# Performance work log

Measured on AMD Instinct MI355X. Metric: run time of the kernel, lower is better.

## Reference

```python
import jax, jax.numpy as jnp
import numpy as np

B, T, C = 8, 2048, 1024
HEAD = 64

def setup_inputs() -> dict:
    key = jax.random.key(0)
    k1, k2, k3, k4 = jax.random.split(key, 4)
    x = jax.random.normal(k1, (B, T, C), dtype=jnp.float32)
    # nn.Linear(n_embed, head_size, bias=False): y = x @ W^T; store as [C, HEAD] for x @ W
    scale = 1.0 / np.sqrt(C)
    Wq = jax.random.normal(k2, (C, HEAD), dtype=jnp.float32) * scale
    Wk = jax.random.normal(k3, (C, HEAD), dtype=jnp.float32) * scale
    Wv = jax.random.normal(k4, (C, HEAD), dtype=jnp.float32) * scale
    return {"x": x, "Wq": Wq, "Wk": Wk, "Wv": Wv}

def reference(x, Wq, Wk, Wv):
    Bx, Tx, Cx = x.shape
    q = x @ Wq            # [B,T,H]
    k = x @ Wk            # [B,T,H]
    v = x @ Wv            # [B,T,H]
    # NOTE: original scales by C**-0.5 (embedding dim), not head_size**-0.5
    aff = jnp.einsum('bqh,bkh->bqk', q, k) * (Cx ** -0.5)  # [B,T,T]
    causal = jnp.tril(jnp.ones((Tx, Tx), dtype=bool))
    aff = jnp.where(causal, aff, -jnp.inf)
    probs = jax.nn.softmax(aff, axis=-1)
    # dropout p=0.0 (eval): identity
    return jnp.einsum('bqk,bkh->bqh', probs, v)
```

## Files before the change

### kernel.cpp

```cpp
#include <hip/hip_runtime.h>
#include <hip/hip_bf16.h>

typedef __attribute__((ext_vector_type(8))) short bf16x8;
typedef __attribute__((ext_vector_type(4))) float f32x4;
typedef __attribute__((ext_vector_type(4))) int i32x4;

#define LOG2E 1.4426950408889634f

static __device__ __forceinline__ unsigned int f2bfu(float f) {
    return (unsigned int)__builtin_bit_cast(unsigned short, __float2bfloat16(f));
}
static __device__ __forceinline__ unsigned int pack2(float lo, float hi) {
    return (f2bfu(hi) << 16) | f2bfu(lo);
}
static __device__ __forceinline__ unsigned short f2bf(float f) {
    return __builtin_bit_cast(unsigned short, __float2bfloat16(f));
}
static __device__ __forceinline__ void gload16(const void* g, void* l) {
    __builtin_amdgcn_global_load_lds(
        (const __attribute__((address_space(1))) unsigned int*)g,
        (__attribute__((address_space(3))) unsigned int*)l,
        16, 0, 0);
}

__global__ __launch_bounds__(256) void wtrans_kernel(
    const float* __restrict__ Wq, const float* __restrict__ Wk,
    const float* __restrict__ Wv, unsigned short* __restrict__ Wts)
{
    const int part = blockIdx.x;
    const int t    = blockIdx.y;
    const int c    = part * 256 + threadIdx.x;
    const int n    = c >> 3;
    const int mat  = n >> 6;
    const int nl   = n & 63;
    const int k0   = t * 64 + (c & 7) * 8;
    const float* W = (mat == 0) ? Wq : ((mat == 1) ? Wk : Wv);
    const float scale = (mat == 0) ? 0.03125f : 1.0f;
    unsigned int s[8];
#pragma unroll
    for (int j = 0; j < 8; ++j)
        s[j] = (unsigned int)f2bf(W[(size_t)(k0 + j) * 64 + nl] * scale);
    i32x4 pk;
    pk[0] = (int)(s[0] | (s[1] << 16));
    pk[1] = (int)(s[2] | (s[3] << 16));
    pk[2] = (int)(s[4] | (s[5] << 16));
    pk[3] = (int)(s[6] | (s[7] << 16));
    *(i32x4*)(Wts + (size_t)t * 12288 + (size_t)c * 8) = pk;
}

__global__ __launch_bounds__(256, 2) void proj_kernel(
    const float* __restrict__ x, const unsigned short* __restrict__ Wts,
    unsigned short* __restrict__ Qb, unsigned short* __restrict__ Kp,
    unsigned short* __restrict__ Vp)
{
    __shared__ __align__(16) unsigned short sA[2][32][72];
    __shared__ __align__(16) unsigned short sBlin[2][12288];
    __shared__ __align__(16) unsigned short sVT[64][48];
    __shared__ __align__(16) unsigned short sK[32][72];

    const int tid  = threadIdx.x;
    const int w    = tid >> 6;
    const int wm   = w >> 1;
    const int wn   = w & 1;
    const int lane = tid & 63;
    const int r    = lane & 15;
    const int g    = lane >> 4;
    const int xv   = r & 7;
    const int mbase = blockIdx.x * 32;

    const int arow = tid >> 3;
    const int acb  = (tid & 7) * 8;
    const float* xptr = x + (size_t)(mbase + arow) * 1024 + acb;

    f32x4 acc[6];
#pragma unroll
    for (int i = 0; i < 6; ++i) acc[i] = (f32x4)0.0f;

    float4 XAa0, XAa1, XAb0, XAb1;

#define LOADX(S0, S1, t_) do { \
        const float* xp = xptr + (size_t)(t_) * 64; \
        S0 = *(const float4*)(xp);  S1 = *(const float4*)(xp + 4); \
    } while (0)

#define GLOADB(t_, buf) do { \
        const unsigned short* wtb = Wts + (size_t)(t_) * 12288; \
        _Pragma("unroll") \
        for (int i = 0; i < 6; ++i) { \
            const int sslot = (w * 6 + i) * 64 + lane; \
            const int ssrc  = sslot ^ ((sslot >> 3) & 7); \
            gload16(wtb + (size_t)ssrc * 8, &sBlin[buf][(size_t)(w * 6 + i) * 512]); \
        } \
    } while (0)

#define STOREA(buf, S0, S1) do { \
        i32x4 pa0 = {(int)pack2(S0.x, S0.y), (int)pack2(S0.z, S0.w), \
                     (int)pack2(S1.x, S1.y), (int)pack2(S1.z, S1.w)}; \
        *(i32x4*)&sA[buf][arow][acb] = pa0; \
    } while (0)

#define COMPSTEP(buf) do { \
        _Pragma("unroll") \
        for (int h = 0; h < 2; ++h) { \
            bf16x8 af = *(const bf16x8*)&sA[buf][wm * 16 + r][h * 32 + g * 8]; \
            _Pragma("unroll") \
            for (int nt = 0; nt < 6; ++nt) { \
                bf16x8 bfr = *(const bf16x8*)&sBlin[buf][ \
                    (size_t)((nt * 2 + wn) * 16 + r) * 64 + (((h * 4 + g) ^ xv) << 3)]; \
                acc[nt] = __builtin_amdgcn_mfma_f32_16x16x32_bf16(af, bfr, acc[nt], 0, 0, 0); \
            } \
        } \
    } while (0)

    GLOADB(0, 0);
    LOADX(XAa0, XAa1, 0);
    LOADX(XAb0, XAb1, 1);
#pragma unroll 1
    for (int t = 0; t < 16; t += 2) {
        STOREA(0, XAa0, XAa1);
        __syncthreads();
        if (t + 2 < 16) LOADX(XAa0, XAa1, t + 2);
        GLOADB(t + 1, 1);
        COMPSTEP(0);
        STOREA(1, XAb0, XAb1);
        __syncthreads();
        if (t + 3 < 16) LOADX(XAb0, XAb1, t + 3);
        if (t + 2 < 16) GLOADB(t + 2, 0);
        COMPSTEP(1);
    }

    const int row0  = mbase + wm * 16 + g * 4;
    const int lrow0 = wm * 16 + g * 4;
#pragma unroll
    for (int nt = 0; nt < 6; ++nt) {
        const int ti  = nt * 2 + wn;
        const int mat = ti >> 2;
        const int col = (ti & 3) * 16 + r;
#pragma unroll
        for (int j = 0; j < 4; ++j) {
            const float v = acc[nt][j];
            if (mat == 0) {
                Qb[(size_t)(row0 + j) * 64 + col] = f2bf(v);
            } else if (mat == 1) {
                sK[lrow0 + j][col] = f2bf(v);
            } else {
                sVT[col][lrow0 + j] = f2bf(v);
            }
        }
    }
    __syncthreads();
    {
        const int bb = mbase >> 11;
        const int tt = (mbase & 2047) >> 5;
        const int f  = tid >> 6;
        const int r2 = lane & 15, g2 = lane >> 4;
        const int krow = 8 * (r2 >> 2) + (r2 & 3) + (f >> 1) * 4;
        const int kcol = (f & 1) * 32 + g2 * 8;
        *(i32x4*)(Kp + ((size_t)(bb * 64 + tt) * 4 + f) * 512 + lane * 8)
            = *(const i32x4*)&sK[krow][kcol];
        *(i32x4*)(Vp + ((size_t)(bb * 64 + tt) * 4 + f) * 512 + lane * 8)
            = *(const i32x4*)&sVT[f * 16 + r2][g2 * 8];
    }
}

__global__ __launch_bounds__(512, 2) void attn_kernel(
    const unsigned short* __restrict__ Qb, const unsigned short* __restrict__ Kp,
    const unsigned short* __restrict__ Vp, float* __restrict__ out)
{
    __shared__ __align__(16) float sO[8][2][4][64][4];
    __shared__ float sM[8][2][16], sL[8][2][16];

    const int tid  = threadIdx.x;
    const int w    = tid >> 6;
    const int lane = tid & 63;
    const int r    = lane & 15;
    const int g    = lane >> 4;
    const int b    = blockIdx.x & 7;
    const int p    = blockIdx.x >> 3;
    const int qbL  = p * 32;
    const int qbH  = 2016 - p * 32;
    const int lastqL = qbL + 31;
    const int lastqH = qbH + 31;

    const unsigned short* Qbb = Qb + (size_t)b * 2048 * 64;
    const unsigned short* Kpb = Kp + (size_t)b * 64 * 2048;
    const unsigned short* Vpb = Vp + (size_t)b * 64 * 2048;

#define QBASE(qs) ((qs) < 2 ? (qbL + (qs) * 16) : (qbH + ((qs) - 2) * 16))

    bf16x8 qf[4][2];
#pragma unroll
    for (int qs = 0; qs < 4; ++qs)
#pragma unroll
        for (int h = 0; h < 2; ++h)
            qf[qs][h] = *(const bf16x8*)(Qbb + (size_t)(QBASE(qs) + r) * 64 + h * 32 + g * 8);

    f32x4 o[4][4];
#pragma unroll
    for (int qs = 0; qs < 4; ++qs)
#pragma unroll
        for (int i = 0; i < 4; ++i) o[qs][i] = (f32x4)0.0f;
    float m[4] = {-1e30f, -1e30f, -1e30f, -1e30f};
    float l[4] = {0.0f, 0.0f, 0.0f, 0.0f};

#define LOADK(K_, kvt) do { \
        const unsigned short* kp = Kpb + (size_t)(kvt) * 2048 + lane * 8; \
        K_[0] = *(const bf16x8*)(kp); \
        K_[1] = *(const bf16x8*)(kp + 512); \
        K_[2] = *(const bf16x8*)(kp + 1024); \
        K_[3] = *(const bf16x8*)(kp + 1536); \
    } while (0)
#define LOADV(V_, kvt) do { \
        const unsigned short* vp = Vpb + (size_t)(kvt) * 2048 + lane * 8; \
        _Pragma("unroll") \
        for (int i = 0; i < 4; ++i) V_[i] = *(const bf16x8*)(vp + i * 512); \
    } while (0)

    bf16x8 KA[4], VA[4];
#pragma unroll 1
    for (int kv0 = w * 32; kv0 <= lastqH; kv0 += 256) {
        const bool doLow = (kv0 <= lastqL);

        LOADK(KA, kv0 >> 5);
        LOADV(VA, kv0 >> 5);

        f32x4 s0[4], s1[4];
        __builtin_amdgcn_s_setprio(1);
#pragma unroll
        for (int qs = 0; qs < 4; ++qs) {
            s0[qs] = (f32x4)0.0f; s1[qs] = (f32x4)0.0f;
            if (qs < 2 && !doLow) continue;
            s0[qs] = __builtin_amdgcn_mfma_f32_16x16x32_bf16(KA[0], qf[qs][0], s0[qs], 0, 0, 0);
            s0[qs] = __builtin_amdgcn_mfma_f32_16x16x32_bf16(KA[1], qf[qs][1], s0[qs], 0, 0, 0);
            s1[qs] = __builtin_amdgcn_mfma_f32_16x16x32_bf16(KA[2], qf[qs][0], s1[qs], 0, 0, 0);
            s1[qs] = __builtin_amdgcn_mfma_f32_16x16x32_bf16(KA[3], qf[qs][1], s1[qs], 0, 0, 0);
        }
        __builtin_amdgcn_s_setprio(0);

        float lm[4] = {-1e30f, -1e30f, -1e30f, -1e30f};
#pragma unroll
        for (int qs = 0; qs < 4; ++qs) {
            if (qs < 2 && !doLow) continue;
            const int q = QBASE(qs) + r;
            if (kv0 + 31 > QBASE(qs)) {
#pragma unroll
                for (int j = 0; j < 4; ++j) {
                    if (kv0 + 8 * g + j > q)     s0[qs][j] = -1e30f;
                    if (kv0 + 8 * g + 4 + j > q) s1[qs][j] = -1e30f;
                }
            }
            lm[qs] = fmaxf(fmaxf(fmaxf(s0[qs][0], s0[qs][1]), fmaxf(s0[qs][2], s0[qs][3])),
                           fmaxf(fmaxf(s1[qs][0], s1[qs][1]), fmaxf(s1[qs][2], s1[qs][3])));
        }
        if (!__all(lm[0] <= m[0] + 8.0f && lm[1] <= m[1] + 8.0f &&
                   lm[2] <= m[2] + 8.0f && lm[3] <= m[3] + 8.0f)) {
#pragma unroll
            for (int qs = 0; qs < 4; ++qs) {
                float t2 = fmaxf(lm[qs], __shfl_xor(lm[qs], 16));
                t2 = fmaxf(t2, __shfl_xor(t2, 32));
                const float mn = fmaxf(m[qs], t2);
                const float alpha = __builtin_amdgcn_exp2f((m[qs] - mn) * LOG2E);
#pragma unroll
                for (int ht = 0; ht < 4; ++ht) o[qs][ht] *= alpha;
                l[qs] *= alpha;
                m[qs] = mn;
            }
        }

        __builtin_amdgcn_s_setprio(1);
#pragma unroll
        for (int qs = 0; qs < 4; ++qs) {
            if (qs < 2 && !doLow) continue;
            float p0[4], p1[4];
#pragma unroll
            for (int j = 0; j < 4; ++j) {
                p0[j] = __builtin_amdgcn_exp2f((s0[qs][j] - m[qs]) * LOG2E);
                p1[j] = __builtin_amdgcn_exp2f((s1[qs][j] - m[qs]) * LOG2E);
                l[qs] += p0[j] + p1[j];
            }
            i32x4 pw;
            pw[0] = (int)pack2(p0[0], p0[1]);
            pw[1] = (int)pack2(p0[2], p0[3]);
            pw[2] = (int)pack2(p1[0], p1[1]);
            pw[3] = (int)pack2(p1[2], p1[3]);
            bf16x8 pfrag = __builtin_bit_cast(bf16x8, pw);
            o[qs][0] = __builtin_amdgcn_mfma_f32_16x16x32_bf16(VA[0], pfrag, o[qs][0], 0, 0, 0);
            o[qs][1] = __builtin_amdgcn_mfma_f32_16x16x32_bf16(VA[1], pfrag, o[qs][1], 0, 0, 0);
            o[qs][2] = __builtin_amdgcn_mfma_f32_16x16x32_bf16(VA[2], pfrag, o[qs][2], 0, 0, 0);
            o[qs][3] = __builtin_amdgcn_mfma_f32_16x16x32_bf16(VA[3], pfrag, o[qs][3], 0, 0, 0);
        }
        __builtin_amdgcn_s_setprio(0);
    }

#define MERGE_STORE(QS, Q2) do { \
        float lr = l[QS]; \
        lr += __shfl_xor(lr, 16); \
        lr += __shfl_xor(lr, 32); \
        if (g == 0) { sM[w][Q2][r] = m[QS]; sL[w][Q2][r] = lr; } \
        _Pragma("unroll") \
        for (int ht = 0; ht < 4; ++ht) *(f32x4*)&sO[w][Q2][ht][lane][0] = o[QS][ht]; \
    } while (0)

#define MERGE_WRITE(QBASE0) do { \
        const int q2 = w >> 2, ht = w & 3; \
        float M = sM[0][q2][r]; \
        _Pragma("unroll") \
        for (int wp = 1; wp < 8; ++wp) M = fmaxf(M, sM[wp][q2][r]); \
        float L = 0.0f; \
        float beta[8]; \
        _Pragma("unroll") \
        for (int wp = 0; wp < 8; ++wp) { \
            beta[wp] = __builtin_amdgcn_exp2f((sM[wp][q2][r] - M) * LOG2E); \
            L += beta[wp] * sL[wp][q2][r]; \
        } \
        f32x4 av = (f32x4)0.0f; \
        _Pragma("unroll") \
        for (int wp = 0; wp < 8; ++wp) { \
            f32x4 t = *(const f32x4*)&sO[wp][q2][ht][lane][0]; \
            av += t * beta[wp]; \
        } \
        const float inv = 1.0f / L; \
        const int qrow = (QBASE0) + q2 * 16 + r; \
        *(f32x4*)(out + ((size_t)b * 2048 + qrow) * 64 + ht * 16 + g * 4) = av * inv; \
    } while (0)

    MERGE_STORE(0, 0);
    MERGE_STORE(1, 1);
    __syncthreads();
    MERGE_WRITE(qbL);
    __syncthreads();
    MERGE_STORE(2, 0);
    MERGE_STORE(3, 1);
    __syncthreads();
    MERGE_WRITE(qbH);
}

extern "C" void kernel_launch(void* const* d_in, const int* in_sizes, int n_in,
                              void* d_out, int out_size, void* d_ws, size_t ws_size,
                              hipStream_t stream) {
    const float* x  = (const float*)d_in[0];
    const float* Wq = (const float*)d_in[1];
    const float* Wk = (const float*)d_in[2];
    const float* Wv = (const float*)d_in[3];
    float* out = (float*)d_out;

    unsigned short* Qb  = (unsigned short*)d_ws;
    unsigned short* Kp  = Qb + (size_t)8 * 2048 * 64;
    unsigned short* Vp  = Kp + (size_t)8 * 64 * 2048;
    unsigned short* Wts = Vp + (size_t)8 * 64 * 2048;

    hipLaunchKernelGGL(wtrans_kernel, dim3(6, 16), dim3(256), 0, stream, Wq, Wk, Wv, Wts);
    hipLaunchKernelGGL(proj_kernel, dim3(512), dim3(256), 0, stream, x, Wts, Qb, Kp, Vp);
    hipLaunchKernelGGL(attn_kernel, dim3(256), dim3(512), 0, stream, Qb, Kp, Vp, out);
}
```

Measured before the change: 41.56 us.

## Split QKV projection across a second grid dimension, one matrix per block

The projection kernel now launches 512x3 blocks, each computing only one of Q, K or V for its 32-row tile. This cuts the per-block weight LDS buffer to a third, reuses it for the K/V staging, and raises launch bounds to allow more resident blocks. The cost is that x is read and converted three times instead of once, trading extra global traffic for more parallelism and occupancy.

```diff
diff --git a/kernel.cpp b/kernel.cpp
--- a/kernel.cpp
+++ b/kernel.cpp
@@ -48,15 +48,13 @@
     *(i32x4*)(Wts + (size_t)t * 12288 + (size_t)c * 8) = pk;
 }
 
-__global__ __launch_bounds__(256, 2) void proj_kernel(
+__global__ __launch_bounds__(256, 6) void proj_kernel(
     const float* __restrict__ x, const unsigned short* __restrict__ Wts,
     unsigned short* __restrict__ Qb, unsigned short* __restrict__ Kp,
     unsigned short* __restrict__ Vp)
 {
     __shared__ __align__(16) unsigned short sA[2][32][72];
-    __shared__ __align__(16) unsigned short sBlin[2][12288];
-    __shared__ __align__(16) unsigned short sVT[64][48];
-    __shared__ __align__(16) unsigned short sK[32][72];
+    __shared__ __align__(16) unsigned short sBlin[2][4096];
 
     const int tid  = threadIdx.x;
     const int w    = tid >> 6;
@@ -65,16 +63,15 @@
     const int lane = tid & 63;
     const int r    = lane & 15;
     const int g    = lane >> 4;
-    const int xv   = r & 7;
     const int mbase = blockIdx.x * 32;
+    const int mat   = blockIdx.y;
 
     const int arow = tid >> 3;
     const int acb  = (tid & 7) * 8;
     const float* xptr = x + (size_t)(mbase + arow) * 1024 + acb;
 
-    f32x4 acc[6];
-#pragma unroll
-    for (int i = 0; i < 6; ++i) acc[i] = (f32x4)0.0f;
+    f32x4 acc[2];
+    acc[0] = (f32x4)0.0f; acc[1] = (f32x4)0.0f;
 
     float4 XAa0, XAa1, XAb0, XAb1;
 
@@ -84,12 +81,13 @@
     } while (0)
 
 #define GLOADB(t_, buf) do { \
-        const unsigned short* wtb = Wts + (size_t)(t_) * 12288; \
-        _Pragma("unroll") \
-        for (int i = 0; i < 6; ++i) { \
-            const int sslot = (w * 6 + i) * 64 + lane; \
-            const int ssrc  = sslot ^ ((sslot >> 3) & 7); \
-            gload16(wtb + (size_t)ssrc * 8, &sBlin[buf][(size_t)(w * 6 + i) * 512]); \
+        const unsigned short* wtb = Wts + (size_t)(t_) * 12288 + (size_t)mat * 4096; \
+        _Pragma("unroll") \
+        for (int i = 0; i < 2; ++i) { \
+            const int c = (w * 2 + i) * 64 + lane; \
+            const int n = c >> 3, sl = c & 7; \
+            gload16(wtb + (size_t)n * 64 + (size_t)(sl ^ (n & 7)) * 8, \
+                    &sBlin[buf][(size_t)(w * 2 + i) * 512]); \
         } \
     } while (0)
 
@@ -104,9 +102,10 @@
         for (int h = 0; h < 2; ++h) { \
             bf16x8 af = *(const bf16x8*)&sA[buf][wm * 16 + r][h * 32 + g * 8]; \
             _Pragma("unroll") \
-            for (int nt = 0; nt < 6; ++nt) { \
+            for (int nt = 0; nt < 2; ++nt) { \
+                const int nl_ = (nt * 2 + wn) * 16 + r; \
                 bf16x8 bfr = *(const bf16x8*)&sBlin[buf][ \
-                    (size_t)((nt * 2 + wn) * 16 + r) * 64 + (((h * 4 + g) ^ xv) << 3)]; \
+                    (size_t)nl_ * 64 + (size_t)(((h * 4 + g) ^ (nl_ & 7)) << 3)]; \
                 acc[nt] = __builtin_amdgcn_mfma_f32_16x16x32_bf16(af, bfr, acc[nt], 0, 0, 0); \
             } \
         } \
@@ -131,35 +130,54 @@
 
     const int row0  = mbase + wm * 16 + g * 4;
     const int lrow0 = wm * 16 + g * 4;
-#pragma unroll
-    for (int nt = 0; nt < 6; ++nt) {
-        const int ti  = nt * 2 + wn;
-        const int mat = ti >> 2;
-        const int col = (ti & 3) * 16 + r;
-#pragma unroll
-        for (int j = 0; j < 4; ++j) {
-            const float v = acc[nt][j];
-            if (mat == 0) {
-                Qb[(size_t)(row0 + j) * 64 + col] = f2bf(v);
-            } else if (mat == 1) {
-                sK[lrow0 + j][col] = f2bf(v);
-            } else {
-                sVT[col][lrow0 + j] = f2bf(v);
-            }
-        }
-    }
-    __syncthreads();
-    {
-        const int bb = mbase >> 11;
-        const int tt = (mbase & 2047) >> 5;
-        const int f  = tid >> 6;
-        const int r2 = lane & 15, g2 = lane >> 4;
-        const int krow = 8 * (r2 >> 2) + (r2 & 3) + (f >> 1) * 4;
-        const int kcol = (f & 1) * 32 + g2 * 8;
-        *(i32x4*)(Kp + ((size_t)(bb * 64 + tt) * 4 + f) * 512 + lane * 8)
-            = *(const i32x4*)&sK[krow][kcol];
-        *(i32x4*)(Vp + ((size_t)(bb * 64 + tt) * 4 + f) * 512 + lane * 8)
-            = *(const i32x4*)&sVT[f * 16 + r2][g2 * 8];
+    if (mat == 0) {
+#pragma unroll
+        for (int nt = 0; nt < 2; ++nt) {
+            const int col = (nt * 2 + wn) * 16 + r;
+#pragma unroll
+            for (int j = 0; j < 4; ++j)
+                Qb[(size_t)(row0 + j) * 64 + col] = f2bf(acc[nt][j]);
+        }
+    } else if (mat == 1) {
+        unsigned short (*sK)[72] = (unsigned short (*)[72])&sBlin[0][0];
+        __syncthreads();
+#pragma unroll
+        for (int nt = 0; nt < 2; ++nt) {
+            const int col = (nt * 2 + wn) * 16 + r;
+#pragma unroll
+            for (int j = 0; j < 4; ++j)
+                sK[lrow0 + j][col] = f2bf(acc[nt][j]);
+        }
+        __syncthreads();
+        {
+            const int bb = mbase >> 11;
+            const int tt = (mbase & 2047) >> 5;
+            const int f  = tid >> 6;
+            const int r2 = lane & 15, g2 = lane >> 4;
+            const int krow = 8 * (r2 >> 2) + (r2 & 3) + (f >> 1) * 4;
+            const int kcol = (f & 1) * 32 + g2 * 8;
+            *(i32x4*)(Kp + ((size_t)(bb * 64 + tt) * 4 + f) * 512 + lane * 8)
+                = *(const i32x4*)&sK[krow][kcol];
+        }
+    } else {
+        unsigned short (*sVT)[48] = (unsigned short (*)[48])&sBlin[0][0];
+        __syncthreads();
+#pragma unroll
+        for (int nt = 0; nt < 2; ++nt) {
+            const int col = (nt * 2 + wn) * 16 + r;
+#pragma unroll
+            for (int j = 0; j < 4; ++j)
+                sVT[col][lrow0 + j] = f2bf(acc[nt][j]);
+        }
+        __syncthreads();
+        {
+            const int bb = mbase >> 11;
+            const int tt = (mbase & 2047) >> 5;
+            const int f  = tid >> 6;
+            const int r2 = lane & 15, g2 = lane >> 4;
+            *(i32x4*)(Vp + ((size_t)(bb * 64 + tt) * 4 + f) * 512 + lane * 8)
+                = *(const i32x4*)&sVT[f * 16 + r2][g2 * 8];
+        }
     }
 }
 
@@ -350,6 +368,6 @@
     unsigned short* Wts = Vp + (size_t)8 * 64 * 2048;
 
     hipLaunchKernelGGL(wtrans_kernel, dim3(6, 16), dim3(256), 0, stream, Wq, Wk, Wv, Wts);
-    hipLaunchKernelGGL(proj_kernel, dim3(512), dim3(256), 0, stream, x, Wts, Qb, Kp, Vp);
+    hipLaunchKernelGGL(proj_kernel, dim3(512, 3), dim3(256), 0, stream, x, Wts, Qb, Kp, Vp);
     hipLaunchKernelGGL(attn_kernel, dim3(256), dim3(512), 0, stream, Qb, Kp, Vp, out);
 }
```

Measured after the change: 48.00 us. 15.5% more time.
